# Kernel optimization log

Measured on AMD Instinct MI355X. Metric: run time of the kernel, lower is better.

Reference implementation:

```python
import jax, jax.numpy as jnp
import numpy as np

DT = 0.01      # timestep
RE = 0.001     # 'Re' coefficient in source
NLEVEL = 5     # multigrid levels
D, H, W = 96, 192, 192  # nz, ny, nx interior grid


def _conv(x, w, stride=1):
    # 1->1 channel 3D stencil conv, VALID padding (matches Conv3d padding=0, bias=0)
    return jax.lax.conv_general_dilated(
        x, w, (stride,) * 3, 'VALID',
        dimension_numbers=('NCDHW', 'OIDHW', 'NCDHW'))


def _pad(x):
    # BC application + halo exchange collapsed to zero halo (single-device reference)
    return jnp.pad(x, ((0, 0), (0, 0), (1, 1), (1, 1), (1, 1)))


def _prol(x):
    # nn.Upsample(scale_factor=2, mode='nearest')
    for ax in (2, 3, 4):
        x = jnp.repeat(x, 2, axis=ax)
    return x


def _stencils():
    wA = np.zeros((1, 1, 3, 3, 3), np.float32)
    wA[0, 0, 1, 1, 1] = -6.0
    for d in range(3):
        idx = [1, 1, 1]
        idx[d] = 0; wA[(0, 0, *idx)] = 1.0
        idx[d] = 2; wA[(0, 0, *idx)] = 1.0
    w_diff = wA.copy()
    w_x = np.zeros((1, 1, 3, 3, 3), np.float32); w_x[0, 0, 1, 1, 0] = -0.5; w_x[0, 0, 1, 1, 2] = 0.5
    w_y = np.zeros((1, 1, 3, 3, 3), np.float32); w_y[0, 0, 1, 0, 1] = -0.5; w_y[0, 0, 1, 2, 1] = 0.5
    w_z = np.zeros((1, 1, 3, 3, 3), np.float32); w_z[0, 0, 0, 1, 1] = -0.5; w_z[0, 0, 2, 1, 1] = 0.5
    w_res = np.full((1, 1, 2, 2, 2), 0.125, np.float32)
    return tuple(jnp.asarray(a) for a in (wA, w_diff, w_x, w_y, w_z, w_res))


def setup_inputs() -> dict:
    key = jax.random.key(0)
    ks = jax.random.split(key, 5)
    shape = (1, 1, D, H, W)
    wA, w_diff, w_xadv, w_yadv, w_zadv, w_res = _stencils()
    return {
        'values_u': jax.random.normal(ks[0], shape, jnp.float32),
        'values_v': jax.random.normal(ks[1], shape, jnp.float32),
        'values_w': jax.random.normal(ks[2], shape, jnp.float32),
        'values_p': jax.random.normal(ks[3], shape, jnp.float32),
        'sigma': jax.random.uniform(ks[4], shape, jnp.float32),
        'wA': wA, 'w_diff': w_diff, 'w_xadv': w_xadv,
        'w_yadv': w_yadv, 'w_zadv': w_zadv, 'w_res': w_res,
        'iteration': 2,
    }


def _forward(values_u, values_v, values_w, values_p, sigma,
             wA, w_diff, w_xadv, w_yadv, w_zadv, w_res, iteration):
    diag = wA[0, 0, 1, 1, 1]
    A = lambda x: _conv(x, wA)
    diff = lambda x: _conv(x, w_diff)
    xadv = lambda x: _conv(x, w_xadv)
    yadv = lambda x: _conv(x, w_yadv)
    zadv = lambda x: _conv(x, w_zadv)
    res = lambda x: _conv(x, w_res, stride=2)

    inv = 1.0 / (1.0 + DT * sigma)           # solid_body (LIBM) damping
    sb = lambda a, b, c: (a * inv, b * inv, c * inv)

    def pg(uu, vv, ww, u, v, w_):
        # PG_vector with k_u = k_v = k_w = ones
        kpp = _pad(jnp.ones_like(u))
        ku = 0.5 * (diff(uu) + diff(uu * kpp) - u * diff(kpp))
        kv = 0.5 * (diff(vv) + diff(vv * kpp) - v * diff(kpp))
        kw = 0.5 * (diff(ww) + diff(ww * kpp) - w_ * diff(kpp))
        return ku, kv, kw

    u, v, w_ = sb(values_u, values_v, values_w)
    uu, vv, ww, pp = _pad(u), _pad(v), _pad(w_), _pad(values_p)

    ku, kv, kw = pg(uu, vv, ww, u, v, w_)
    b_u = u + 0.5 * (RE * ku * DT - u * xadv(uu) * DT - v * yadv(uu) * DT - w_ * zadv(uu) * DT) - xadv(pp) * DT
    b_v = v + 0.5 * (RE * kv * DT - u * xadv(vv) * DT - v * yadv(vv) * DT - w_ * zadv(vv) * DT) - yadv(pp) * DT
    b_w = w_ + 0.5 * (RE * kw * DT - u * xadv(ww) * DT - v * yadv(ww) * DT - w_ * zadv(ww) * DT) - zadv(pp) * DT
    b_u, b_v, b_w = sb(b_u, b_v, b_w)
    buu, bvv, bww = _pad(b_u), _pad(b_v), _pad(b_w)

    ku, kv, kw = pg(buu, bvv, bww, b_u, b_v, b_w)
    u = u + RE * ku * DT - b_u * xadv(buu) * DT - b_v * yadv(buu) * DT - b_w * zadv(buu) * DT - xadv(pp) * DT
    v = v + RE * kv * DT - b_u * xadv(bvv) * DT - b_v * yadv(bvv) * DT - b_w * zadv(bvv) * DT - yadv(pp) * DT
    w_ = w_ + RE * kw * DT - b_u * xadv(bww) * DT - b_v * yadv(bww) * DT - b_w * zadv(bww) * DT - zadv(pp) * DT
    u, v, w_ = sb(u, v, w_)
    uu, vv, ww = _pad(u), _pad(v), _pad(w_)

    # F_cycle_MG: multigrid pressure solve
    b = -(xadv(uu) + yadv(vv) + zadv(ww)) / DT
    p = values_p
    for _ in range(iteration):
        wmg = jnp.zeros((1, 1, 1, 1, 1), p.dtype)
        r = A(pp) - b
        r_s = [r]
        for _i in range(1, NLEVEL - 1):
            r = res(r)
            r_s.append(r)
        for i in reversed(range(1, NLEVEL - 1)):
            wmg = wmg - A(_pad(wmg)) / diag + r_s[i] / diag  # Jacobi smooth (broadcasts at coarsest)
            wmg = _prol(wmg)
        p = p - wmg
        p = p - A(pp) / diag + b / diag
        pp = _pad(p)

    u = u - xadv(pp) * DT
    v = v - yadv(pp) * DT
    w_ = w_ - zadv(pp) * DT
    u, v, w_ = sb(u, v, w_)
    return u, v, w_, p, wmg, r


def reference(values_u, values_v, values_w, values_p, sigma,
              wA, w_diff, w_xadv, w_yadv, w_zadv, w_res, iteration):
    return _forward(values_u, values_v, values_w, values_p, sigma,
                    wA, w_diff, w_xadv, w_yadv, w_zadv, w_res, iteration)
```

## Files before the change

kernel.cpp:

```cpp
#include <hip/hip_runtime.h>

#define DZc 96
#define HYc 192
#define WXc 192
#define SHs (WXc)
#define SDs (HYc*WXc)
#define NTOT (DZc*HYc*WXc)
#define DTc 0.01f
#define REc 0.001f

#define D1 48
#define H1 96
#define W1 96
#define N1 (D1*H1*W1)
#define D2 24
#define H2 48
#define W2 48
#define N2 (D2*H2*W2)
#define D3 12
#define H3 24
#define W3 24
#define N3 (D3*H3*W3)

struct Nbr {
  int c, xm, xp, ym, yp, zm, zp;
  float mxm,mxp,mym,myp,mzm,mzp;
  float m;
};
__device__ __forceinline__ Nbr mknbr(int x,int y,int z){
  Nbr n;
  int idx = (z*HYc + y)*WXc + x;
  bool hxm=x>0, hxp=x<WXc-1, hym=y>0, hyp=y<HYc-1, hzm=z>0, hzp=z<DZc-1;
  n.c = idx;
  n.xm = hxm ? idx-1   : idx;  n.xp = hxp ? idx+1   : idx;
  n.ym = hym ? idx-SHs : idx;  n.yp = hyp ? idx+SHs : idx;
  n.zm = hzm ? idx-SDs : idx;  n.zp = hzp ? idx+SDs : idx;
  n.mxm = hxm?1.f:0.f; n.mxp = hxp?1.f:0.f;
  n.mym = hym?1.f:0.f; n.myp = hyp?1.f:0.f;
  n.mzm = hzm?1.f:0.f; n.mzp = hzp?1.f:0.f;
  n.m = 6.f - (n.mxm+n.mxp+n.mym+n.myp+n.mzm+n.mzp);
  return n;
}

__global__ __launch_bounds__(256) void k_pred(
    const float* __restrict__ vu, const float* __restrict__ vv,
    const float* __restrict__ vw, const float* __restrict__ sig,
    const float* __restrict__ p,
    float* __restrict__ bu, float* __restrict__ bv, float* __restrict__ bw){
  int x = blockIdx.x*64 + threadIdx.x;
  int y = blockIdx.y*4  + threadIdx.y;
  int z = blockIdx.z;
  Nbr n = mknbr(x,y,z);

  float sc  = sig[n.c],  sxm = sig[n.xm], sxp = sig[n.xp];
  float sym = sig[n.ym], syp = sig[n.yp], szm = sig[n.zm], szp = sig[n.zp];
  float auc = vu[n.c],  auxm = vu[n.xm], auxp = vu[n.xp];
  float auym= vu[n.ym], auyp = vu[n.yp], auzm = vu[n.zm], auzp = vu[n.zp];
  float avc = vv[n.c],  avxm = vv[n.xm], avxp = vv[n.xp];
  float avym= vv[n.ym], avyp = vv[n.yp], avzm = vv[n.zm], avzp = vv[n.zp];
  float awc = vw[n.c],  awxm = vw[n.xm], awxp = vw[n.xp];
  float awym= vw[n.ym], awyp = vw[n.yp], awzm = vw[n.zm], awzp = vw[n.zp];
  float pxm = p[n.xm]*n.mxm, pxp = p[n.xp]*n.mxp;
  float pym = p[n.ym]*n.mym, pyp = p[n.yp]*n.myp;
  float pzm = p[n.zm]*n.mzm, pzp = p[n.zp]*n.mzp;

  float ivc  = 1.f/(1.f + DTc*sc);
  float ivxm = 1.f/(1.f + DTc*sxm), ivxp = 1.f/(1.f + DTc*sxp);
  float ivym = 1.f/(1.f + DTc*sym), ivyp = 1.f/(1.f + DTc*syp);
  float ivzm = 1.f/(1.f + DTc*szm), ivzp = 1.f/(1.f + DTc*szp);

  float uc  = auc*ivc;
  float uxm = auxm*ivxm*n.mxm, uxp = auxp*ivxp*n.mxp;
  float uym = auym*ivym*n.mym, uyp = auyp*ivyp*n.myp;
  float uzm = auzm*ivzm*n.mzm, uzp = auzp*ivzp*n.mzp;
  float vc  = avc*ivc;
  float vxm = avxm*ivxm*n.mxm, vxp = avxp*ivxp*n.mxp;
  float vym = avym*ivym*n.mym, vyp = avyp*ivyp*n.myp;
  float vzm = avzm*ivzm*n.mzm, vzp = avzp*ivzp*n.mzp;
  float wc  = awc*ivc;
  float wxm = awxm*ivxm*n.mxm, wxp = awxp*ivxp*n.mxp;
  float wym = awym*ivym*n.mym, wyp = awyp*ivyp*n.myp;
  float wzm = awzm*ivzm*n.mzm, wzp = awzp*ivzp*n.mzp;

  float ku = (uxm+uxp+uym+uyp+uzm+uzp - 6.f*uc) + 0.5f*n.m*uc;
  float kv = (vxm+vxp+vym+vyp+vzm+vzp - 6.f*vc) + 0.5f*n.m*vc;
  float kw = (wxm+wxp+wym+wyp+wzm+wzp - 6.f*wc) + 0.5f*n.m*wc;

  float advu = uc*0.5f*(uxp-uxm) + vc*0.5f*(uyp-uym) + wc*0.5f*(uzp-uzm);
  float advv = uc*0.5f*(vxp-vxm) + vc*0.5f*(vyp-vym) + wc*0.5f*(vzp-vzm);
  float advw = uc*0.5f*(wxp-wxm) + vc*0.5f*(wyp-wym) + wc*0.5f*(wzp-wzm);

  float bu_ = uc + 0.5f*(REc*ku*DTc - advu*DTc) - 0.5f*(pxp-pxm)*DTc;
  float bv_ = vc + 0.5f*(REc*kv*DTc - advv*DTc) - 0.5f*(pyp-pym)*DTc;
  float bw_ = wc + 0.5f*(REc*kw*DTc - advw*DTc) - 0.5f*(pzp-pzm)*DTc;

  bu[n.c] = bu_*ivc;
  bv[n.c] = bv_*ivc;
  bw[n.c] = bw_*ivc;
}

__global__ __launch_bounds__(256) void k_corr(
    const float* __restrict__ bu, const float* __restrict__ bv,
    const float* __restrict__ bw, const float* __restrict__ p,
    const float* __restrict__ vu, const float* __restrict__ vv,
    const float* __restrict__ vw, const float* __restrict__ sig,
    float* __restrict__ u, float* __restrict__ v, float* __restrict__ w){
  int x = blockIdx.x*64 + threadIdx.x;
  int y = blockIdx.y*4  + threadIdx.y;
  int z = blockIdx.z;
  Nbr n = mknbr(x,y,z);

  float buc = bu[n.c];
  float buxm = bu[n.xm]*n.mxm, buxp = bu[n.xp]*n.mxp;
  float buym = bu[n.ym]*n.mym, buyp = bu[n.yp]*n.myp;
  float buzm = bu[n.zm]*n.mzm, buzp = bu[n.zp]*n.mzp;
  float bvc = bv[n.c];
  float bvxm = bv[n.xm]*n.mxm, bvxp = bv[n.xp]*n.mxp;
  float bvym = bv[n.ym]*n.mym, bvyp = bv[n.yp]*n.myp;
  float bvzm = bv[n.zm]*n.mzm, bvzp = bv[n.zp]*n.mzp;
  float bwc = bw[n.c];
  float bwxm = bw[n.xm]*n.mxm, bwxp = bw[n.xp]*n.mxp;
  float bwym = bw[n.ym]*n.mym, bwyp = bw[n.yp]*n.myp;
  float bwzm = bw[n.zm]*n.mzm, bwzp = bw[n.zp]*n.mzp;
  float pxm = p[n.xm]*n.mxm, pxp = p[n.xp]*n.mxp;
  float pym = p[n.ym]*n.mym, pyp = p[n.yp]*n.myp;
  float pzm = p[n.zm]*n.mzm, pzp = p[n.zp]*n.mzp;
  float uc0 = vu[n.c], vc0 = vv[n.c], wc0 = vw[n.c], sc = sig[n.c];

  float ivc = 1.f/(1.f + DTc*sc);

  float ku = (buxm+buxp+buym+buyp+buzm+buzp - 6.f*buc) + 0.5f*n.m*buc;
  float kv = (bvxm+bvxp+bvym+bvyp+bvzm+bvzp - 6.f*bvc) + 0.5f*n.m*bvc;
  float kw = (bwxm+bwxp+bwym+bwyp+bwzm+bwzp - 6.f*bwc) + 0.5f*n.m*bwc;

  float advu = buc*0.5f*(buxp-buxm) + bvc*0.5f*(buyp-buym) + bwc*0.5f*(buzp-buzm);
  float advv = buc*0.5f*(bvxp-bvxm) + bvc*0.5f*(bvyp-bvym) + bwc*0.5f*(bvzp-bvzm);
  float advw = buc*0.5f*(bwxp-bwxm) + bvc*0.5f*(bwyp-bwym) + bwc*0.5f*(bwzp-bwzm);

  float u1 = uc0*ivc + REc*ku*DTc - advu*DTc - 0.5f*(pxp-pxm)*DTc;
  float v1 = vc0*ivc + REc*kv*DTc - advv*DTc - 0.5f*(pyp-pym)*DTc;
  float w1 = wc0*ivc + REc*kw*DTc - advw*DTc - 0.5f*(pzp-pzm)*DTc;

  u[n.c] = u1*ivc; v[n.c] = v1*ivc; w[n.c] = w1*ivc;
}

#define RESTRICT_BODY(rv, r1p, r2p)                                           \
  __shared__ float l0[4][4][16];                                              \
  __shared__ float l1[2][2][8];                                               \
  l0[threadIdx.z][threadIdx.y][threadIdx.x] = (rv);                           \
  __syncthreads();                                                            \
  {                                                                           \
    int t = (threadIdx.z*4 + threadIdx.y)*16 + threadIdx.x;                   \
    if (t < 32){                                                              \
      int xc = t & 7, yc = (t>>3)&1, zc = (t>>4)&1;                           \
      float s = 0.f;                                                          \
      for (int a=0;a<2;a++) for (int bq=0;bq<2;bq++) for (int c=0;c<2;c++)    \
        s += l0[2*zc+a][2*yc+bq][2*xc+c];                                     \
      float r1v = 0.125f*s;                                                   \
      int X = blockIdx.x*8+xc, Y = blockIdx.y*2+yc, Z = blockIdx.z*2+zc;      \
      (r1p)[(Z*H1+Y)*W1+X] = r1v;                                             \
      l1[zc][yc][xc] = r1v;                                                   \
    }                                                                         \
    __syncthreads();                                                          \
    if (t < 4){                                                               \
      float s = 0.f;                                                          \
      for (int a=0;a<2;a++) for (int bq=0;bq<2;bq++) for (int c=0;c<2;c++)    \
        s += l1[a][bq][2*t+c];                                                \
      int X = blockIdx.x*4+t, Y = blockIdx.y, Z = blockIdx.z;                 \
      (r2p)[(Z*H2+Y)*W2+X] = 0.125f*s;                                        \
    }                                                                         \
  }

__global__ __launch_bounds__(256) void k_res1(
    const float* __restrict__ u, const float* __restrict__ v,
    const float* __restrict__ w, const float* __restrict__ p,
    float* __restrict__ bdiv, float* __restrict__ r0,
    float* __restrict__ r1, float* __restrict__ r2){
  int x = blockIdx.x*16 + threadIdx.x;
  int y = blockIdx.y*4  + threadIdx.y;
  int z = blockIdx.z*4  + threadIdx.z;
  Nbr n = mknbr(x,y,z);

  float uxm = u[n.xm]*n.mxm, uxp = u[n.xp]*n.mxp;
  float vym = v[n.ym]*n.mym, vyp = v[n.yp]*n.myp;
  float wzm = w[n.zm]*n.mzm, wzp = w[n.zp]*n.mzp;
  float pc  = p[n.c];
  float pxm = p[n.xm]*n.mxm, pxp = p[n.xp]*n.mxp;
  float pym = p[n.ym]*n.mym, pyp = p[n.yp]*n.myp;
  float pzm = p[n.zm]*n.mzm, pzp = p[n.zp]*n.mzp;

  float b = -(0.5f*(uxp-uxm) + 0.5f*(vyp-vym) + 0.5f*(wzp-wzm)) * (1.f/DTc);
  float lap = pxm+pxp+pym+pyp+pzm+pzp - 6.f*pc;
  float rv = lap - b;
  bdiv[n.c] = b;
  r0[n.c] = rv;
  RESTRICT_BODY(rv, r1, r2)
}

__global__ __launch_bounds__(256) void k_res2(
    const float* __restrict__ vp, const float* __restrict__ r0,
    const float* __restrict__ w1, const float* __restrict__ b,
    float* __restrict__ p1, float* __restrict__ r0b,
    float* __restrict__ r1b, float* __restrict__ r2b){
  int x = blockIdx.x*16 + threadIdx.x;
  int y = blockIdx.y*4  + threadIdx.y;
  int z = blockIdx.z*4  + threadIdx.z;
  Nbr n = mknbr(x,y,z);
  int xm = (x>0)?x-1:0, xp = (x<WXc-1)?x+1:x;
  int ym = (y>0)?y-1:0, yp = (y<HYc-1)?y+1:y;
  int zm = (z>0)?z-1:0, zp = (z<DZc-1)?z+1:z;

  #define CI(qz,qy,qx) ((((qz)>>1)*H1 + ((qy)>>1))*W1 + ((qx)>>1))
  float pc  = vp[n.c]  - w1[CI(z,y,x)]   + r0[n.c]*(1.f/6.f);
  float pxm = (vp[n.xm] - w1[CI(z,y,xm)] + r0[n.xm]*(1.f/6.f))*n.mxm;
  float pxp = (vp[n.xp] - w1[CI(z,y,xp)] + r0[n.xp]*(1.f/6.f))*n.mxp;
  float pym = (vp[n.ym] - w1[CI(z,ym,x)] + r0[n.ym]*(1.f/6.f))*n.mym;
  float pyp = (vp[n.yp] - w1[CI(z,yp,x)] + r0[n.yp]*(1.f/6.f))*n.myp;
  float pzm = (vp[n.zm] - w1[CI(zm,y,x)] + r0[n.zm]*(1.f/6.f))*n.mzm;
  float pzp = (vp[n.zp] - w1[CI(zp,y,x)] + r0[n.zp]*(1.f/6.f))*n.mzp;
  #undef CI

  float lap = pxm+pxp+pym+pyp+pzm+pzp - 6.f*pc;
  float rv = lap - b[n.c];
  p1[n.c] = pc;
  r0b[n.c] = rv;
  RESTRICT_BODY(rv, r1b, r2b)
}

__global__ void k_lvl2(const float* __restrict__ r2, float* __restrict__ w2o,
                       float* __restrict__ r3o){
  int idx = blockIdx.x*256 + threadIdx.x;
  if (idx >= N2) return;
  int x = idx % W2; int tt = idx / W2; int y = tt % H2; int z = tt / H2;
  int cx = x>>1, cy = y>>1, cz = z>>1;
  auto r3eval = [&](int az,int ay,int ax)->float{
    int fi = ((2*az)*H2 + 2*ay)*W2 + 2*ax;
    return 0.125f*(r2[fi] + r2[fi+1] + r2[fi+W2] + r2[fi+W2+1]
                 + r2[fi+H2*W2] + r2[fi+H2*W2+1] + r2[fi+H2*W2+W2] + r2[fi+H2*W2+W2+1]);
  };
  float mxm=(x>0)?1.f:0.f, mxp=(x<W2-1)?1.f:0.f;
  float mym=(y>0)?1.f:0.f, myp=(y<H2-1)?1.f:0.f;
  float mzm=(z>0)?1.f:0.f, mzp=(z<D2-1)?1.f:0.f;
  int cxm=(x>0)?(x-1)>>1:0, cxp=(x<W2-1)?(x+1)>>1:cx;
  int cym=(y>0)?(y-1)>>1:0, cyp=(y<H2-1)?(y+1)>>1:cy;
  int czm=(z>0)?(z-1)>>1:0, czp=(z<D2-1)?(z+1)>>1:cz;
  const float k6 = -1.f/6.f;
  float r3c = r3eval(cz,cy,cx);
  float tc  = r3c*k6;
  float txm = r3eval(cz,cy,cxm)*k6*mxm, txp = r3eval(cz,cy,cxp)*k6*mxp;
  float tym = r3eval(cz,cym,cx)*k6*mym, typ = r3eval(cz,cyp,cx)*k6*myp;
  float tzm = r3eval(czm,cy,cx)*k6*mzm, tzp = r3eval(czp,cy,cx)*k6*mzp;
  float lapt = txm+txp+tym+typ+tzm+tzp - 6.f*tc;
  w2o[idx] = tc + lapt*(1.f/6.f) - r2[idx]*(1.f/6.f);
  if (((x|y|z)&1)==0) r3o[(cz*H3+cy)*W3+cx] = r3c;
}

__global__ void k_lvl1(const float* __restrict__ w2, const float* __restrict__ r1,
                       float* __restrict__ w1o){
  int idx = blockIdx.x*256 + threadIdx.x;
  if (idx >= N1) return;
  int x = idx % W1; int tt = idx / W1; int y = tt % H1; int z = tt / H1;
  int cx = x>>1, cy = y>>1, cz = z>>1;
  float mxm=(x>0)?1.f:0.f, mxp=(x<W1-1)?1.f:0.f;
  float mym=(y>0)?1.f:0.f, myp=(y<H1-1)?1.f:0.f;
  float mzm=(z>0)?1.f:0.f, mzp=(z<D1-1)?1.f:0.f;
  int cxm=(x>0)?(x-1)>>1:0, cxp=(x<W1-1)?(x+1)>>1:cx;
  int cym=(y>0)?(y-1)>>1:0, cyp=(y<H1-1)?(y+1)>>1:cy;
  int czm=(z>0)?(z-1)>>1:0, czp=(z<D1-1)?(z+1)>>1:cz;
  auto A = [&](int az,int ay,int ax)->float{ return w2[(az*H2+ay)*W2+ax]; };
  float tc = A(cz,cy,cx);
  float txm = A(cz,cy,cxm)*mxm, txp = A(cz,cy,cxp)*mxp;
  float tym = A(cz,cym,cx)*mym, typ = A(cz,cyp,cx)*myp;
  float tzm = A(czm,cy,cx)*mzm, tzp = A(czp,cy,cx)*mzp;
  float lapt = txm+txp+tym+typ+tzm+tzp - 6.f*tc;
  w1o[idx] = tc + lapt*(1.f/6.f) - r1[idx]*(1.f/6.f);
}

__global__ __launch_bounds__(256) void k_final(
    const float* __restrict__ p1, const float* __restrict__ r0b,
    const float* __restrict__ w1b,
    const float* __restrict__ u, const float* __restrict__ v,
    const float* __restrict__ w, const float* __restrict__ sig,
    float* __restrict__ ou, float* __restrict__ ov, float* __restrict__ ow,
    float* __restrict__ op, float* __restrict__ owmg){
  int x = blockIdx.x*64 + threadIdx.x;
  int y = blockIdx.y*4  + threadIdx.y;
  int z = blockIdx.z;
  Nbr n = mknbr(x,y,z);
  int xm = (x>0)?x-1:0, xp = (x<WXc-1)?x+1:x;
  int ym = (y>0)?y-1:0, yp = (y<HYc-1)?y+1:y;
  int zm = (z>0)?z-1:0, zp = (z<DZc-1)?z+1:z;

  #define CI(qz,qy,qx) ((((qz)>>1)*H1 + ((qy)>>1))*W1 + ((qx)>>1))
  float wmc = w1b[CI(z,y,x)];
  float pc  = p1[n.c] - wmc + r0b[n.c]*(1.f/6.f);
  float pxm = (p1[n.xm] - w1b[CI(z,y,xm)] + r0b[n.xm]*(1.f/6.f))*n.mxm;
  float pxp = (p1[n.xp] - w1b[CI(z,y,xp)] + r0b[n.xp]*(1.f/6.f))*n.mxp;
  float pym = (p1[n.ym] - w1b[CI(z,ym,x)] + r0b[n.ym]*(1.f/6.f))*n.mym;
  float pyp = (p1[n.yp] - w1b[CI(z,yp,x)] + r0b[n.yp]*(1.f/6.f))*n.myp;
  float pzm = (p1[n.zm] - w1b[CI(zm,y,x)] + r0b[n.zm]*(1.f/6.f))*n.mzm;
  float pzp = (p1[n.zp] - w1b[CI(zp,y,x)] + r0b[n.zp]*(1.f/6.f))*n.mzp;
  #undef CI

  float iv = 1.f/(1.f + DTc*sig[n.c]);
  op[n.c]   = pc;
  owmg[n.c] = wmc;
  ou[n.c] = (u[n.c] - 0.5f*(pxp-pxm)*DTc)*iv;
  ov[n.c] = (v[n.c] - 0.5f*(pyp-pym)*DTc)*iv;
  ow[n.c] = (w[n.c] - 0.5f*(pzp-pzm)*DTc)*iv;
}

extern "C" void kernel_launch(void* const* d_in, const int* in_sizes, int n_in,
                              void* d_out, int out_size, void* d_ws, size_t ws_size,
                              hipStream_t stream){
  const float* vu  = (const float*)d_in[0];
  const float* vv  = (const float*)d_in[1];
  const float* vw  = (const float*)d_in[2];
  const float* vp  = (const float*)d_in[3];
  const float* sig = (const float*)d_in[4];

  const size_t N = (size_t)NTOT;
  float* ws   = (float*)d_ws;
  float* u    = ws;
  float* v    = ws + N;
  float* w    = ws + 2*N;
  float* bu   = ws + 3*N;
  float* bv   = ws + 4*N;
  float* bw   = ws + 5*N;
  float* r0b  = ws + 6*N;
  float* r1   = ws + 7*N;
  float* r2   = r1 + N1;
  float* w2   = r2 + N2;
  float* w1   = w2 + N2;

  float* out     = (float*)d_out;
  float* out_u   = out;
  float* out_v   = out + N;
  float* out_w   = out + 2*N;
  float* out_p   = out + 3*N;
  float* out_wmg = out + 4*N;
  float* out_r   = out + 5*N;

  dim3 bA(64,4,1), gA(WXc/64, HYc/4, DZc);
  dim3 bR(16,4,4), gR(WXc/16, HYc/4, DZc/4);

  k_pred<<<gA,bA,0,stream>>>(vu,vv,vw,sig,vp,bu,bv,bw);
  k_corr<<<gA,bA,0,stream>>>(bu,bv,bw,vp,vu,vv,vw,sig,u,v,w);

  float* bdiv = bu; float* r0 = bv; float* p1 = bw;
  k_res1<<<gR,bR,0,stream>>>(u,v,w,vp,bdiv,r0,r1,r2);
  k_lvl2<<<(N2+255)/256,256,0,stream>>>(r2,w2,out_r);
  k_lvl1<<<(N1+255)/256,256,0,stream>>>(w2,r1,w1);

  k_res2<<<gR,bR,0,stream>>>(vp,r0,w1,bdiv,p1,r0b,r1,r2);
  k_lvl2<<<(N2+255)/256,256,0,stream>>>(r2,w2,out_r);
  k_lvl1<<<(N1+255)/256,256,0,stream>>>(w2,r1,w1);

  k_final<<<gA,bA,0,stream>>>(p1,r0b,w1,u,v,w,sig,out_u,out_v,out_w,out_p,out_wmg);
}
```

Before: 295.2 us.

## Vectorize stencil kernels to four x-points per thread and drop bdiv buffer

Each thread in the predictor, corrector, residual and final kernels now handles four consecutive x points. It loads the centre row and the y/z neighbours as float4 and writes float4 results, with only scalar x-halo loads. In the second residual pass the divergence buffer is removed by rewriting r = A(p - w) - b as r0 + lap(r0)/6 - lap(w), so one full-grid read and write disappear. Restriction now uses full-row 192-wide shared tiles in 768-thread blocks. The intent is fewer memory transactions and less redundant neighbour traffic, at the cost of higher register pressure and fewer, larger blocks.

```diff
diff --git a/kernel.cpp b/kernel.cpp
--- a/kernel.cpp
+++ b/kernel.cpp
@@ -22,209 +22,258 @@
 #define W3 24
 #define N3 (D3*H3*W3)
 
-struct Nbr {
-  int c, xm, xp, ym, yp, zm, zp;
-  float mxm,mxp,mym,myp,mzm,mzp;
-  float m;
+
+struct Row6 { float a[6]; };
+
+struct Geo {
+  int base, il, ir, iym, iyp, izm, izp;
+  float mxl, mxr, mym, myp, mzm, mzp;
 };
-__device__ __forceinline__ Nbr mknbr(int x,int y,int z){
-  Nbr n;
-  int idx = (z*HYc + y)*WXc + x;
-  bool hxm=x>0, hxp=x<WXc-1, hym=y>0, hyp=y<HYc-1, hzm=z>0, hzp=z<DZc-1;
-  n.c = idx;
-  n.xm = hxm ? idx-1   : idx;  n.xp = hxp ? idx+1   : idx;
-  n.ym = hym ? idx-SHs : idx;  n.yp = hyp ? idx+SHs : idx;
-  n.zm = hzm ? idx-SDs : idx;  n.zp = hzp ? idx+SDs : idx;
-  n.mxm = hxm?1.f:0.f; n.mxp = hxp?1.f:0.f;
-  n.mym = hym?1.f:0.f; n.myp = hyp?1.f:0.f;
-  n.mzm = hzm?1.f:0.f; n.mzp = hzp?1.f:0.f;
-  n.m = 6.f - (n.mxm+n.mxp+n.mym+n.myp+n.mzm+n.mzp);
-  return n;
-}
-
-__global__ __launch_bounds__(256) void k_pred(
+
+__device__ __forceinline__ Geo mkgeo(int x0,int y,int z){
+  Geo g;
+  g.base = (z*HYc + y)*WXc + x0;
+  bool hxm=x0>0, hxp=x0<WXc-4, hym=y>0, hyp=y<HYc-1, hzm=z>0, hzp=z<DZc-1;
+  g.il  = hxm ? g.base-1   : g.base;  g.ir  = hxp ? g.base+4   : g.base;
+  g.iym = hym ? g.base-SHs : g.base;  g.iyp = hyp ? g.base+SHs : g.base;
+  g.izm = hzm ? g.base-SDs : g.base;  g.izp = hzp ? g.base+SDs : g.base;
+  g.mxl = hxm?1.f:0.f; g.mxr = hxp?1.f:0.f;
+  g.mym = hym?1.f:0.f; g.myp = hyp?1.f:0.f;
+  g.mzm = hzm?1.f:0.f; g.mzp = hzp?1.f:0.f;
+  return g;
+}
+
+__device__ __forceinline__ Row6 ld6(const float* __restrict__ f, const Geo& g){
+  Row6 r;
+  float4 c = *reinterpret_cast<const float4*>(f + g.base);
+  r.a[0]=f[g.il]*g.mxl; r.a[1]=c.x; r.a[2]=c.y; r.a[3]=c.z; r.a[4]=c.w; r.a[5]=f[g.ir]*g.mxr;
+  return r;
+}
+__device__ __forceinline__ void ld4a(const float* __restrict__ f, int idx, float* o){
+  float4 c = *reinterpret_cast<const float4*>(f + idx);
+  o[0]=c.x; o[1]=c.y; o[2]=c.z; o[3]=c.w;
+}
+
+struct Sten { Row6 c; float ym[4], yp[4], zm[4], zp[4]; };
+__device__ __forceinline__ Sten ldsten(const float* __restrict__ f, const Geo& g){
+  Sten s;
+  s.c = ld6(f,g);
+  ld4a(f,g.iym,s.ym); ld4a(f,g.iyp,s.yp); ld4a(f,g.izm,s.zm); ld4a(f,g.izp,s.zp);
+  return s;
+}
+
+__device__ __forceinline__ void restrict_body(
+    const float rv[4], int x0,
+    float (*l0)[4][192], float (*l1)[2][96],
+    float* __restrict__ r1p, float* __restrict__ r2p,
+    int by, int bz){
+  *reinterpret_cast<float4*>(&l0[threadIdx.z][threadIdx.y][x0]) =
+      make_float4(rv[0],rv[1],rv[2],rv[3]);
+  __syncthreads();
+  int t = (threadIdx.z*4 + threadIdx.y)*48 + threadIdx.x;
+  if (t < 384){
+    int xc = t % 96, yc = (t/96)&1, zc = t/192;
+    float s = 0.f;
+    for (int a=0;a<2;a++)
+      for (int bq=0;bq<2;bq++)
+        s += l0[2*zc+a][2*yc+bq][2*xc] + l0[2*zc+a][2*yc+bq][2*xc+1];
+    float r1v = 0.125f*s;
+    r1p[((bz*2+zc)*H1 + (by*2+yc))*W1 + xc] = r1v;
+    l1[zc][yc][xc] = r1v;
+  }
+  __syncthreads();
+  if (t < 48){
+    float s = 0.f;
+    for (int a=0;a<2;a++)
+      for (int bq=0;bq<2;bq++)
+        s += l1[a][bq][2*t] + l1[a][bq][2*t+1];
+    r2p[(bz*H2 + by)*W2 + t] = 0.125f*s;
+  }
+}
+
+__global__ __launch_bounds__(192) void k_pred(
     const float* __restrict__ vu, const float* __restrict__ vv,
     const float* __restrict__ vw, const float* __restrict__ sig,
     const float* __restrict__ p,
     float* __restrict__ bu, float* __restrict__ bv, float* __restrict__ bw){
-  int x = blockIdx.x*64 + threadIdx.x;
-  int y = blockIdx.y*4  + threadIdx.y;
-  int z = blockIdx.z;
-  Nbr n = mknbr(x,y,z);
-
-  float sc  = sig[n.c],  sxm = sig[n.xm], sxp = sig[n.xp];
-  float sym = sig[n.ym], syp = sig[n.yp], szm = sig[n.zm], szp = sig[n.zp];
-  float auc = vu[n.c],  auxm = vu[n.xm], auxp = vu[n.xp];
-  float auym= vu[n.ym], auyp = vu[n.yp], auzm = vu[n.zm], auzp = vu[n.zp];
-  float avc = vv[n.c],  avxm = vv[n.xm], avxp = vv[n.xp];
-  float avym= vv[n.ym], avyp = vv[n.yp], avzm = vv[n.zm], avzp = vv[n.zp];
-  float awc = vw[n.c],  awxm = vw[n.xm], awxp = vw[n.xp];
-  float awym= vw[n.ym], awyp = vw[n.yp], awzm = vw[n.zm], awzp = vw[n.zp];
-  float pxm = p[n.xm]*n.mxm, pxp = p[n.xp]*n.mxp;
-  float pym = p[n.ym]*n.mym, pyp = p[n.yp]*n.myp;
-  float pzm = p[n.zm]*n.mzm, pzp = p[n.zp]*n.mzp;
-
-  float ivc  = 1.f/(1.f + DTc*sc);
-  float ivxm = 1.f/(1.f + DTc*sxm), ivxp = 1.f/(1.f + DTc*sxp);
-  float ivym = 1.f/(1.f + DTc*sym), ivyp = 1.f/(1.f + DTc*syp);
-  float ivzm = 1.f/(1.f + DTc*szm), ivzp = 1.f/(1.f + DTc*szp);
-
-  float uc  = auc*ivc;
-  float uxm = auxm*ivxm*n.mxm, uxp = auxp*ivxp*n.mxp;
-  float uym = auym*ivym*n.mym, uyp = auyp*ivyp*n.myp;
-  float uzm = auzm*ivzm*n.mzm, uzp = auzp*ivzp*n.mzp;
-  float vc  = avc*ivc;
-  float vxm = avxm*ivxm*n.mxm, vxp = avxp*ivxp*n.mxp;
-  float vym = avym*ivym*n.mym, vyp = avyp*ivyp*n.myp;
-  float vzm = avzm*ivzm*n.mzm, vzp = avzp*ivzp*n.mzp;
-  float wc  = awc*ivc;
-  float wxm = awxm*ivxm*n.mxm, wxp = awxp*ivxp*n.mxp;
-  float wym = awym*ivym*n.mym, wyp = awyp*ivyp*n.myp;
-  float wzm = awzm*ivzm*n.mzm, wzp = awzp*ivzp*n.mzp;
-
-  float ku = (uxm+uxp+uym+uyp+uzm+uzp - 6.f*uc) + 0.5f*n.m*uc;
-  float kv = (vxm+vxp+vym+vyp+vzm+vzp - 6.f*vc) + 0.5f*n.m*vc;
-  float kw = (wxm+wxp+wym+wyp+wzm+wzp - 6.f*wc) + 0.5f*n.m*wc;
-
-  float advu = uc*0.5f*(uxp-uxm) + vc*0.5f*(uyp-uym) + wc*0.5f*(uzp-uzm);
-  float advv = uc*0.5f*(vxp-vxm) + vc*0.5f*(vyp-vym) + wc*0.5f*(vzp-vzm);
-  float advw = uc*0.5f*(wxp-wxm) + vc*0.5f*(wyp-wym) + wc*0.5f*(wzp-wzm);
-
-  float bu_ = uc + 0.5f*(REc*ku*DTc - advu*DTc) - 0.5f*(pxp-pxm)*DTc;
-  float bv_ = vc + 0.5f*(REc*kv*DTc - advv*DTc) - 0.5f*(pyp-pym)*DTc;
-  float bw_ = wc + 0.5f*(REc*kw*DTc - advw*DTc) - 0.5f*(pzp-pzm)*DTc;
-
-  bu[n.c] = bu_*ivc;
-  bv[n.c] = bv_*ivc;
-  bw[n.c] = bw_*ivc;
-}
-
-__global__ __launch_bounds__(256) void k_corr(
+  int x0 = threadIdx.x*4, y = blockIdx.y*4 + threadIdx.y, z = blockIdx.z;
+  Geo g = mkgeo(x0,y,z);
+
+  Sten S = ldsten(sig,g);
+  Sten U = ldsten(vu,g);
+  Sten V = ldsten(vv,g);
+  Sten W = ldsten(vw,g);
+  Sten P = ldsten(p,g);
+
+  float iv6[6], du6[6], dv6[6], dw6[6];
+  #pragma unroll
+  for (int i=0;i<6;i++){
+    iv6[i] = 1.f/(1.f + DTc*S.c.a[i]);
+    du6[i] = U.c.a[i]*iv6[i]; dv6[i] = V.c.a[i]*iv6[i]; dw6[i] = W.c.a[i]*iv6[i];
+  }
+  float duym[4],duyp[4],duzm[4],duzp[4];
+  float dvym[4],dvyp[4],dvzm[4],dvzp[4];
+  float dwym[4],dwyp[4],dwzm[4],dwzp[4];
+  #pragma unroll
+  for (int e=0;e<4;e++){
+    float iym = g.mym/(1.f + DTc*S.ym[e]);
+    float iyp = g.myp/(1.f + DTc*S.yp[e]);
+    float izm = g.mzm/(1.f + DTc*S.zm[e]);
+    float izp = g.mzp/(1.f + DTc*S.zp[e]);
+    duym[e]=U.ym[e]*iym; duyp[e]=U.yp[e]*iyp; duzm[e]=U.zm[e]*izm; duzp[e]=U.zp[e]*izp;
+    dvym[e]=V.ym[e]*iym; dvyp[e]=V.yp[e]*iyp; dvzm[e]=V.zm[e]*izm; dvzp[e]=V.zp[e]*izp;
+    dwym[e]=W.ym[e]*iym; dwyp[e]=W.yp[e]*iyp; dwzm[e]=W.zm[e]*izm; dwzp[e]=W.zp[e]*izp;
+  }
+
+  float rbu[4], rbv[4], rbw[4];
+  #pragma unroll
+  for (int e=0;e<4;e++){
+    const float exm = (e==0)?g.mxl:1.f, exp_ = (e==3)?g.mxr:1.f;
+    const float me = (1.f-exm)+(1.f-exp_)+(1.f-g.mym)+(1.f-g.myp)+(1.f-g.mzm)+(1.f-g.mzp);
+    float uc=du6[e+1], vc=dv6[e+1], wc=dw6[e+1];
+    float ku = (du6[e]+du6[e+2]+duym[e]+duyp[e]+duzm[e]+duzp[e] - 6.f*uc) + 0.5f*me*uc;
+    float kv = (dv6[e]+dv6[e+2]+dvym[e]+dvyp[e]+dvzm[e]+dvzp[e] - 6.f*vc) + 0.5f*me*vc;
+    float kw = (dw6[e]+dw6[e+2]+dwym[e]+dwyp[e]+dwzm[e]+dwzp[e] - 6.f*wc) + 0.5f*me*wc;
+    float advu = uc*0.5f*(du6[e+2]-du6[e]) + vc*0.5f*(duyp[e]-duym[e]) + wc*0.5f*(duzp[e]-duzm[e]);
+    float advv = uc*0.5f*(dv6[e+2]-dv6[e]) + vc*0.5f*(dvyp[e]-dvym[e]) + wc*0.5f*(dvzp[e]-dvzm[e]);
+    float advw = uc*0.5f*(dw6[e+2]-dw6[e]) + vc*0.5f*(dwyp[e]-dwym[e]) + wc*0.5f*(dwzp[e]-dwzm[e]);
+    float gpx = 0.5f*(P.c.a[e+2]-P.c.a[e]);
+    float gpy = 0.5f*(P.yp[e]*g.myp - P.ym[e]*g.mym);
+    float gpz = 0.5f*(P.zp[e]*g.mzp - P.zm[e]*g.mzm);
+    rbu[e] = (uc + 0.5f*(REc*ku*DTc - advu*DTc) - gpx*DTc)*iv6[e+1];
+    rbv[e] = (vc + 0.5f*(REc*kv*DTc - advv*DTc) - gpy*DTc)*iv6[e+1];
+    rbw[e] = (wc + 0.5f*(REc*kw*DTc - advw*DTc) - gpz*DTc)*iv6[e+1];
+  }
+  *reinterpret_cast<float4*>(bu+g.base) = make_float4(rbu[0],rbu[1],rbu[2],rbu[3]);
+  *reinterpret_cast<float4*>(bv+g.base) = make_float4(rbv[0],rbv[1],rbv[2],rbv[3]);
+  *reinterpret_cast<float4*>(bw+g.base) = make_float4(rbw[0],rbw[1],rbw[2],rbw[3]);
+}
+
+__global__ __launch_bounds__(192) void k_corr(
     const float* __restrict__ bu, const float* __restrict__ bv,
     const float* __restrict__ bw, const float* __restrict__ p,
     const float* __restrict__ vu, const float* __restrict__ vv,
     const float* __restrict__ vw, const float* __restrict__ sig,
     float* __restrict__ u, float* __restrict__ v, float* __restrict__ w){
-  int x = blockIdx.x*64 + threadIdx.x;
-  int y = blockIdx.y*4  + threadIdx.y;
-  int z = blockIdx.z;
-  Nbr n = mknbr(x,y,z);
-
-  float buc = bu[n.c];
-  float buxm = bu[n.xm]*n.mxm, buxp = bu[n.xp]*n.mxp;
-  float buym = bu[n.ym]*n.mym, buyp = bu[n.yp]*n.myp;
-  float buzm = bu[n.zm]*n.mzm, buzp = bu[n.zp]*n.mzp;
-  float bvc = bv[n.c];
-  float bvxm = bv[n.xm]*n.mxm, bvxp = bv[n.xp]*n.mxp;
-  float bvym = bv[n.ym]*n.mym, bvyp = bv[n.yp]*n.myp;
-  float bvzm = bv[n.zm]*n.mzm, bvzp = bv[n.zp]*n.mzp;
-  float bwc = bw[n.c];
-  float bwxm = bw[n.xm]*n.mxm, bwxp = bw[n.xp]*n.mxp;
-  float bwym = bw[n.ym]*n.mym, bwyp = bw[n.yp]*n.myp;
-  float bwzm = bw[n.zm]*n.mzm, bwzp = bw[n.zp]*n.mzp;
-  float pxm = p[n.xm]*n.mxm, pxp = p[n.xp]*n.mxp;
-  float pym = p[n.ym]*n.mym, pyp = p[n.yp]*n.myp;
-  float pzm = p[n.zm]*n.mzm, pzp = p[n.zp]*n.mzp;
-  float uc0 = vu[n.c], vc0 = vv[n.c], wc0 = vw[n.c], sc = sig[n.c];
-
-  float ivc = 1.f/(1.f + DTc*sc);
-
-  float ku = (buxm+buxp+buym+buyp+buzm+buzp - 6.f*buc) + 0.5f*n.m*buc;
-  float kv = (bvxm+bvxp+bvym+bvyp+bvzm+bvzp - 6.f*bvc) + 0.5f*n.m*bvc;
-  float kw = (bwxm+bwxp+bwym+bwyp+bwzm+bwzp - 6.f*bwc) + 0.5f*n.m*bwc;
-
-  float advu = buc*0.5f*(buxp-buxm) + bvc*0.5f*(buyp-buym) + bwc*0.5f*(buzp-buzm);
-  float advv = buc*0.5f*(bvxp-bvxm) + bvc*0.5f*(bvyp-bvym) + bwc*0.5f*(bvzp-bvzm);
-  float advw = buc*0.5f*(bwxp-bwxm) + bvc*0.5f*(bwyp-bwym) + bwc*0.5f*(bwzp-bwzm);
-
-  float u1 = uc0*ivc + REc*ku*DTc - advu*DTc - 0.5f*(pxp-pxm)*DTc;
-  float v1 = vc0*ivc + REc*kv*DTc - advv*DTc - 0.5f*(pyp-pym)*DTc;
-  float w1 = wc0*ivc + REc*kw*DTc - advw*DTc - 0.5f*(pzp-pzm)*DTc;
-
-  u[n.c] = u1*ivc; v[n.c] = v1*ivc; w[n.c] = w1*ivc;
-}
-
-#define RESTRICT_BODY(rv, r1p, r2p)                                           \
-  __shared__ float l0[4][4][16];                                              \
-  __shared__ float l1[2][2][8];                                               \
-  l0[threadIdx.z][threadIdx.y][threadIdx.x] = (rv);                           \
-  __syncthreads();                                                            \
-  {                                                                           \
-    int t = (threadIdx.z*4 + threadIdx.y)*16 + threadIdx.x;                   \
-    if (t < 32){                                                              \
-      int xc = t & 7, yc = (t>>3)&1, zc = (t>>4)&1;                           \
-      float s = 0.f;                                                          \
-      for (int a=0;a<2;a++) for (int bq=0;bq<2;bq++) for (int c=0;c<2;c++)    \
-        s += l0[2*zc+a][2*yc+bq][2*xc+c];                                     \
-      float r1v = 0.125f*s;                                                   \
-      int X = blockIdx.x*8+xc, Y = blockIdx.y*2+yc, Z = blockIdx.z*2+zc;      \
-      (r1p)[(Z*H1+Y)*W1+X] = r1v;                                             \
-      l1[zc][yc][xc] = r1v;                                                   \
-    }                                                                         \
-    __syncthreads();                                                          \
-    if (t < 4){                                                               \
-      float s = 0.f;                                                          \
-      for (int a=0;a<2;a++) for (int bq=0;bq<2;bq++) for (int c=0;c<2;c++)    \
-        s += l1[a][bq][2*t+c];                                                \
-      int X = blockIdx.x*4+t, Y = blockIdx.y, Z = blockIdx.z;                 \
-      (r2p)[(Z*H2+Y)*W2+X] = 0.125f*s;                                        \
-    }                                                                         \
-  }
-
-__global__ __launch_bounds__(256) void k_res1(
+  int x0 = threadIdx.x*4, y = blockIdx.y*4 + threadIdx.y, z = blockIdx.z;
+  Geo g = mkgeo(x0,y,z);
+
+  Sten BU = ldsten(bu,g);
+  Sten BV = ldsten(bv,g);
+  Sten BW = ldsten(bw,g);
+  Sten P  = ldsten(p,g);
+  float cu[4],cv[4],cw[4],cs[4];
+  ld4a(vu,g.base,cu); ld4a(vv,g.base,cv); ld4a(vw,g.base,cw); ld4a(sig,g.base,cs);
+
+  float ru[4], rv[4], rw[4];
+  #pragma unroll
+  for (int e=0;e<4;e++){
+    const float exm = (e==0)?g.mxl:1.f, exp_ = (e==3)?g.mxr:1.f;
+    const float me = (1.f-exm)+(1.f-exp_)+(1.f-g.mym)+(1.f-g.myp)+(1.f-g.mzm)+(1.f-g.mzp);
+    float ivc = 1.f/(1.f + DTc*cs[e]);
+    float buc=BU.c.a[e+1], bvc=BV.c.a[e+1], bwc=BW.c.a[e+1];
+    float buym=BU.ym[e]*g.mym, buyp=BU.yp[e]*g.myp, buzm=BU.zm[e]*g.mzm, buzp=BU.zp[e]*g.mzp;
+    float bvym=BV.ym[e]*g.mym, bvyp=BV.yp[e]*g.myp, bvzm=BV.zm[e]*g.mzm, bvzp=BV.zp[e]*g.mzp;
+    float bwym=BW.ym[e]*g.mym, bwyp=BW.yp[e]*g.myp, bwzm=BW.zm[e]*g.mzm, bwzp=BW.zp[e]*g.mzp;
+    float ku = (BU.c.a[e]+BU.c.a[e+2]+buym+buyp+buzm+buzp - 6.f*buc) + 0.5f*me*buc;
+    float kv = (BV.c.a[e]+BV.c.a[e+2]+bvym+bvyp+bvzm+bvzp - 6.f*bvc) + 0.5f*me*bvc;
+    float kw = (BW.c.a[e]+BW.c.a[e+2]+bwym+bwyp+bwzm+bwzp - 6.f*bwc) + 0.5f*me*bwc;
+    float advu = buc*0.5f*(BU.c.a[e+2]-BU.c.a[e]) + bvc*0.5f*(buyp-buym) + bwc*0.5f*(buzp-buzm);
+    float advv = buc*0.5f*(BV.c.a[e+2]-BV.c.a[e]) + bvc*0.5f*(bvyp-bvym) + bwc*0.5f*(bvzp-bvzm);
+    float advw = buc*0.5f*(BW.c.a[e+2]-BW.c.a[e]) + bvc*0.5f*(bwyp-bwym) + bwc*0.5f*(bwzp-bwzm);
+    float gpx = 0.5f*(P.c.a[e+2]-P.c.a[e]);
+    float gpy = 0.5f*(P.yp[e]*g.myp - P.ym[e]*g.mym);
+    float gpz = 0.5f*(P.zp[e]*g.mzp - P.zm[e]*g.mzm);
+    ru[e] = (cu[e]*ivc + REc*ku*DTc - advu*DTc - gpx*DTc)*ivc;
+    rv[e] = (cv[e]*ivc + REc*kv*DTc - advv*DTc - gpy*DTc)*ivc;
+    rw[e] = (cw[e]*ivc + REc*kw*DTc - advw*DTc - gpz*DTc)*ivc;
+  }
+  *reinterpret_cast<float4*>(u+g.base) = make_float4(ru[0],ru[1],ru[2],ru[3]);
+  *reinterpret_cast<float4*>(v+g.base) = make_float4(rv[0],rv[1],rv[2],rv[3]);
+  *reinterpret_cast<float4*>(w+g.base) = make_float4(rw[0],rw[1],rw[2],rw[3]);
+}
+
+__global__ __launch_bounds__(768) void k_res1(
     const float* __restrict__ u, const float* __restrict__ v,
     const float* __restrict__ w, const float* __restrict__ p,
-    float* __restrict__ bdiv, float* __restrict__ r0,
-    float* __restrict__ r1, float* __restrict__ r2){
-  int x = blockIdx.x*16 + threadIdx.x;
-  int y = blockIdx.y*4  + threadIdx.y;
-  int z = blockIdx.z*4  + threadIdx.z;
-  Nbr n = mknbr(x,y,z);
-
-  float uxm = u[n.xm]*n.mxm, uxp = u[n.xp]*n.mxp;
-  float vym = v[n.ym]*n.mym, vyp = v[n.yp]*n.myp;
-  float wzm = w[n.zm]*n.mzm, wzp = w[n.zp]*n.mzp;
-  float pc  = p[n.c];
-  float pxm = p[n.xm]*n.mxm, pxp = p[n.xp]*n.mxp;
-  float pym = p[n.ym]*n.mym, pyp = p[n.yp]*n.myp;
-  float pzm = p[n.zm]*n.mzm, pzp = p[n.zp]*n.mzp;
-
-  float b = -(0.5f*(uxp-uxm) + 0.5f*(vyp-vym) + 0.5f*(wzp-wzm)) * (1.f/DTc);
-  float lap = pxm+pxp+pym+pyp+pzm+pzp - 6.f*pc;
-  float rv = lap - b;
-  bdiv[n.c] = b;
-  r0[n.c] = rv;
-  RESTRICT_BODY(rv, r1, r2)
-}
-
-__global__ __launch_bounds__(256) void k_res2(
+    float* __restrict__ r0, float* __restrict__ r1, float* __restrict__ r2){
+  __shared__ float l0[4][4][192];
+  __shared__ float l1[2][2][96];
+  int x0 = threadIdx.x*4;
+  int y = blockIdx.y*4 + threadIdx.y;
+  int z = blockIdx.z*4 + threadIdx.z;
+  Geo g = mkgeo(x0,y,z);
+
+  Row6 u6 = ld6(u,g);
+  float vym[4],vyp[4],wzm[4],wzp[4];
+  ld4a(v,g.iym,vym); ld4a(v,g.iyp,vyp); ld4a(w,g.izm,wzm); ld4a(w,g.izp,wzp);
+  Sten P = ldsten(p,g);
+
+  float rv[4];
+  #pragma unroll
+  for (int e=0;e<4;e++){
+    float b = -(0.5f*(u6.a[e+2]-u6.a[e])
+              + 0.5f*(vyp[e]*g.myp - vym[e]*g.mym)
+              + 0.5f*(wzp[e]*g.mzp - wzm[e]*g.mzm)) * (1.f/DTc);
+    float lap = P.c.a[e]+P.c.a[e+2]
+              + P.ym[e]*g.mym + P.yp[e]*g.myp + P.zm[e]*g.mzm + P.zp[e]*g.mzp
+              - 6.f*P.c.a[e+1];
+    rv[e] = lap - b;
+  }
+  *reinterpret_cast<float4*>(r0+g.base) = make_float4(rv[0],rv[1],rv[2],rv[3]);
+  restrict_body(rv, x0, l0, l1, r1, r2, blockIdx.y, blockIdx.z);
+}
+
+__global__ __launch_bounds__(768) void k_res2(
     const float* __restrict__ vp, const float* __restrict__ r0,
-    const float* __restrict__ w1, const float* __restrict__ b,
+    const float* __restrict__ w1,
     float* __restrict__ p1, float* __restrict__ r0b,
     float* __restrict__ r1b, float* __restrict__ r2b){
-  int x = blockIdx.x*16 + threadIdx.x;
-  int y = blockIdx.y*4  + threadIdx.y;
-  int z = blockIdx.z*4  + threadIdx.z;
-  Nbr n = mknbr(x,y,z);
-  int xm = (x>0)?x-1:0, xp = (x<WXc-1)?x+1:x;
-  int ym = (y>0)?y-1:0, yp = (y<HYc-1)?y+1:y;
-  int zm = (z>0)?z-1:0, zp = (z<DZc-1)?z+1:z;
-
-  #define CI(qz,qy,qx) ((((qz)>>1)*H1 + ((qy)>>1))*W1 + ((qx)>>1))
-  float pc  = vp[n.c]  - w1[CI(z,y,x)]   + r0[n.c]*(1.f/6.f);
-  float pxm = (vp[n.xm] - w1[CI(z,y,xm)] + r0[n.xm]*(1.f/6.f))*n.mxm;
-  float pxp = (vp[n.xp] - w1[CI(z,y,xp)] + r0[n.xp]*(1.f/6.f))*n.mxp;
-  float pym = (vp[n.ym] - w1[CI(z,ym,x)] + r0[n.ym]*(1.f/6.f))*n.mym;
-  float pyp = (vp[n.yp] - w1[CI(z,yp,x)] + r0[n.yp]*(1.f/6.f))*n.myp;
-  float pzm = (vp[n.zm] - w1[CI(zm,y,x)] + r0[n.zm]*(1.f/6.f))*n.mzm;
-  float pzp = (vp[n.zp] - w1[CI(zp,y,x)] + r0[n.zp]*(1.f/6.f))*n.mzp;
-  #undef CI
-
-  float lap = pxm+pxp+pym+pyp+pzm+pzp - 6.f*pc;
-  float rv = lap - b[n.c];
-  p1[n.c] = pc;
-  r0b[n.c] = rv;
-  RESTRICT_BODY(rv, r1b, r2b)
+  __shared__ float l0[4][4][192];
+  __shared__ float l1[2][2][96];
+  int x0 = threadIdx.x*4;
+  int y = blockIdx.y*4 + threadIdx.y;
+  int z = blockIdx.z*4 + threadIdx.z;
+  Geo g = mkgeo(x0,y,z);
+
+  Sten R = ldsten(r0,g);
+  float vpa[4]; ld4a(vp,g.base,vpa);
+
+  int cz=z>>1, cy=y>>1, cx0=x0>>1;
+  const float* wrow = w1 + (cz*H1+cy)*W1;
+  int icxm = (x0>0)? cx0-1 : cx0;
+  int icxp = (x0<WXc-4)? cx0+2 : cx0+1;
+  float wc0=wrow[icxm], wc1=wrow[cx0], wc2=wrow[cx0+1], wc3=wrow[icxp];
+  int cym_=(y>0)?((y-1)>>1):cy, cyp_=(y<HYc-1)?((y+1)>>1):cy;
+  int czm_=(z>0)?((z-1)>>1):cz, czp_=(z<DZc-1)?((z+1)>>1):cz;
+  const float* rym_r = w1 + (cz*H1+cym_)*W1;
+  const float* ryp_r = w1 + (cz*H1+cyp_)*W1;
+  const float* rzm_r = w1 + (czm_*H1+cy)*W1;
+  const float* rzp_r = w1 + (czp_*H1+cy)*W1;
+  float wym0=rym_r[cx0], wym1=rym_r[cx0+1];
+  float wyp0=ryp_r[cx0], wyp1=ryp_r[cx0+1];
+  float wzm0=rzm_r[cx0], wzm1=rzm_r[cx0+1];
+  float wzp0=rzp_r[cx0], wzp1=rzp_r[cx0+1];
+
+  float rv[4], pv[4];
+  #pragma unroll
+  for (int e=0;e<4;e++){
+    const float exm = (e==0)?g.mxl:1.f, exp_ = (e==3)?g.mxr:1.f;
+    float tc  = (e<2)? wc1 : wc2;
+    float txm = ((e==0)? wc0 : (e<3)? wc1 : wc2)*exm;
+    float txp = ((e==0)? wc1 : (e<3)? wc2 : wc3)*exp_;
+    float tym = ((e<2)? wym0 : wym1)*g.mym, typ = ((e<2)? wyp0 : wyp1)*g.myp;
+    float tzm = ((e<2)? wzm0 : wzm1)*g.mzm, tzp = ((e<2)? wzp0 : wzp1)*g.mzp;
+    float lapw = txm+txp+tym+typ+tzm+tzp - 6.f*tc;
+    float lapr = R.c.a[e]+R.c.a[e+2]
+               + R.ym[e]*g.mym + R.yp[e]*g.myp + R.zm[e]*g.mzm + R.zp[e]*g.mzp
+               - 6.f*R.c.a[e+1];
+    rv[e] = R.c.a[e+1] + lapr*(1.f/6.f) - lapw;
+    pv[e] = vpa[e] - tc + R.c.a[e+1]*(1.f/6.f);
+  }
+  *reinterpret_cast<float4*>(p1 +g.base) = make_float4(pv[0],pv[1],pv[2],pv[3]);
+  *reinterpret_cast<float4*>(r0b+g.base) = make_float4(rv[0],rv[1],rv[2],rv[3]);
+  restrict_body(rv, x0, l0, l1, r1b, r2b, blockIdx.y, blockIdx.z);
 }
 
 __global__ void k_lvl2(const float* __restrict__ r2, float* __restrict__ w2o,
@@ -276,38 +325,65 @@
   w1o[idx] = tc + lapt*(1.f/6.f) - r1[idx]*(1.f/6.f);
 }
 
-__global__ __launch_bounds__(256) void k_final(
+__global__ __launch_bounds__(192) void k_final(
     const float* __restrict__ p1, const float* __restrict__ r0b,
     const float* __restrict__ w1b,
     const float* __restrict__ u, const float* __restrict__ v,
     const float* __restrict__ w, const float* __restrict__ sig,
     float* __restrict__ ou, float* __restrict__ ov, float* __restrict__ ow,
     float* __restrict__ op, float* __restrict__ owmg){
-  int x = blockIdx.x*64 + threadIdx.x;
-  int y = blockIdx.y*4  + threadIdx.y;
-  int z = blockIdx.z;
-  Nbr n = mknbr(x,y,z);
-  int xm = (x>0)?x-1:0, xp = (x<WXc-1)?x+1:x;
-  int ym = (y>0)?y-1:0, yp = (y<HYc-1)?y+1:y;
-  int zm = (z>0)?z-1:0, zp = (z<DZc-1)?z+1:z;
-
-  #define CI(qz,qy,qx) ((((qz)>>1)*H1 + ((qy)>>1))*W1 + ((qx)>>1))
-  float wmc = w1b[CI(z,y,x)];
-  float pc  = p1[n.c] - wmc + r0b[n.c]*(1.f/6.f);
-  float pxm = (p1[n.xm] - w1b[CI(z,y,xm)] + r0b[n.xm]*(1.f/6.f))*n.mxm;
-  float pxp = (p1[n.xp] - w1b[CI(z,y,xp)] + r0b[n.xp]*(1.f/6.f))*n.mxp;
-  float pym = (p1[n.ym] - w1b[CI(z,ym,x)] + r0b[n.ym]*(1.f/6.f))*n.mym;
-  float pyp = (p1[n.yp] - w1b[CI(z,yp,x)] + r0b[n.yp]*(1.f/6.f))*n.myp;
-  float pzm = (p1[n.zm] - w1b[CI(zm,y,x)] + r0b[n.zm]*(1.f/6.f))*n.mzm;
-  float pzp = (p1[n.zp] - w1b[CI(zp,y,x)] + r0b[n.zp]*(1.f/6.f))*n.mzp;
-  #undef CI
-
-  float iv = 1.f/(1.f + DTc*sig[n.c]);
-  op[n.c]   = pc;
-  owmg[n.c] = wmc;
-  ou[n.c] = (u[n.c] - 0.5f*(pxp-pxm)*DTc)*iv;
-  ov[n.c] = (v[n.c] - 0.5f*(pyp-pym)*DTc)*iv;
-  ow[n.c] = (w[n.c] - 0.5f*(pzp-pzm)*DTc)*iv;
+  int x0 = threadIdx.x*4, y = blockIdx.y*4 + threadIdx.y, z = blockIdx.z;
+  Geo g = mkgeo(x0,y,z);
+
+  Sten P = ldsten(p1,g);
+  Sten R = ldsten(r0b,g);
+  float cu[4],cv[4],cw[4],cs[4];
+  ld4a(u,g.base,cu); ld4a(v,g.base,cv); ld4a(w,g.base,cw); ld4a(sig,g.base,cs);
+
+  int cz=z>>1, cy=y>>1, cx0=x0>>1;
+  const float* wrow = w1b + (cz*H1+cy)*W1;
+  int icxm = (x0>0)? cx0-1 : cx0;
+  int icxp = (x0<WXc-4)? cx0+2 : cx0+1;
+  float wc0=wrow[icxm], wc1=wrow[cx0], wc2=wrow[cx0+1], wc3=wrow[icxp];
+  int cym_=(y>0)?((y-1)>>1):cy, cyp_=(y<HYc-1)?((y+1)>>1):cy;
+  int czm_=(z>0)?((z-1)>>1):cz, czp_=(z<DZc-1)?((z+1)>>1):cz;
+  const float* rym_r = w1b + (cz*H1+cym_)*W1;
+  const float* ryp_r = w1b + (cz*H1+cyp_)*W1;
+  const float* rzm_r = w1b + (czm_*H1+cy)*W1;
+  const float* rzp_r = w1b + (czp_*H1+cy)*W1;
+  float wym0=rym_r[cx0], wym1=rym_r[cx0+1];
+  float wyp0=ryp_r[cx0], wyp1=ryp_r[cx0+1];
+  float wzm0=rzm_r[cx0], wzm1=rzm_r[cx0+1];
+  float wzp0=rzp_r[cx0], wzp1=rzp_r[cx0+1];
+
+  float rou[4], rov[4], row_[4], rop[4], rowm[4];
+  #pragma unroll
+  for (int e=0;e<4;e++){
+    const float exm = (e==0)?g.mxl:1.f, exp_ = (e==3)?g.mxr:1.f;
+    float tc  = (e<2)? wc1 : wc2;
+    float txm = (e==0)? wc0 : (e<3)? wc1 : wc2;
+    float txp = (e==0)? wc1 : (e<3)? wc2 : wc3;
+    float tym = (e<2)? wym0 : wym1, typ = (e<2)? wyp0 : wyp1;
+    float tzm = (e<2)? wzm0 : wzm1, tzp = (e<2)? wzp0 : wzp1;
+    float p2xm = (P.c.a[e]   + R.c.a[e]  *(1.f/6.f) - txm)*exm;
+    float p2xp = (P.c.a[e+2] + R.c.a[e+2]*(1.f/6.f) - txp)*exp_;
+    float p2ym = (P.ym[e] + R.ym[e]*(1.f/6.f) - tym)*g.mym;
+    float p2yp = (P.yp[e] + R.yp[e]*(1.f/6.f) - typ)*g.myp;
+    float p2zm = (P.zm[e] + R.zm[e]*(1.f/6.f) - tzm)*g.mzm;
+    float p2zp = (P.zp[e] + R.zp[e]*(1.f/6.f) - tzp)*g.mzp;
+    float pc = P.c.a[e+1] - tc + R.c.a[e+1]*(1.f/6.f);
+    float iv = 1.f/(1.f + DTc*cs[e]);
+    rop[e]  = pc;
+    rowm[e] = tc;
+    rou[e] = (cu[e] - 0.5f*(p2xp-p2xm)*DTc)*iv;
+    rov[e] = (cv[e] - 0.5f*(p2yp-p2ym)*DTc)*iv;
+    row_[e]= (cw[e] - 0.5f*(p2zp-p2zm)*DTc)*iv;
+  }
+  *reinterpret_cast<float4*>(ou+g.base)   = make_float4(rou[0],rou[1],rou[2],rou[3]);
+  *reinterpret_cast<float4*>(ov+g.base)   = make_float4(rov[0],rov[1],rov[2],rov[3]);
+  *reinterpret_cast<float4*>(ow+g.base)   = make_float4(row_[0],row_[1],row_[2],row_[3]);
+  *reinterpret_cast<float4*>(op+g.base)   = make_float4(rop[0],rop[1],rop[2],rop[3]);
+  *reinterpret_cast<float4*>(owmg+g.base) = make_float4(rowm[0],rowm[1],rowm[2],rowm[3]);
 }
 
 extern "C" void kernel_launch(void* const* d_in, const int* in_sizes, int n_in,
@@ -341,18 +417,18 @@
   float* out_wmg = out + 4*N;
   float* out_r   = out + 5*N;
 
-  dim3 bA(64,4,1), gA(WXc/64, HYc/4, DZc);
-  dim3 bR(16,4,4), gR(WXc/16, HYc/4, DZc/4);
+  dim3 bA(48,4,1), gA(1, HYc/4, DZc);
+  dim3 bR(48,4,4), gR(1, HYc/4, DZc/4);
 
   k_pred<<<gA,bA,0,stream>>>(vu,vv,vw,sig,vp,bu,bv,bw);
   k_corr<<<gA,bA,0,stream>>>(bu,bv,bw,vp,vu,vv,vw,sig,u,v,w);
 
-  float* bdiv = bu; float* r0 = bv; float* p1 = bw;
-  k_res1<<<gR,bR,0,stream>>>(u,v,w,vp,bdiv,r0,r1,r2);
+  float* r0 = bv; float* p1 = bw;
+  k_res1<<<gR,bR,0,stream>>>(u,v,w,vp,r0,r1,r2);
   k_lvl2<<<(N2+255)/256,256,0,stream>>>(r2,w2,out_r);
   k_lvl1<<<(N1+255)/256,256,0,stream>>>(w2,r1,w1);
 
-  k_res2<<<gR,bR,0,stream>>>(vp,r0,w1,bdiv,p1,r0b,r1,r2);
+  k_res2<<<gR,bR,0,stream>>>(vp,r0,w1,p1,r0b,r1,r2);
   k_lvl2<<<(N2+255)/256,256,0,stream>>>(r2,w2,out_r);
   k_lvl1<<<(N1+255)/256,256,0,stream>>>(w2,r1,w1);
 
```

New measurement: 247.0 us. 16.3% less time.
